# Optimization experiments

Hardware: AMD Instinct MI355X
Metric: run time of the kernel (lower is better)

Reference implementation:

```python
import jax, jax.numpy as jnp
import numpy as np

B, N, M, D = 16, 1024, 1024, 768


def setup_inputs() -> dict:
    key = jax.random.key(0)
    k1, k2, k3, k4, k5 = jax.random.split(key, 5)
    inp = jax.random.normal(k1, (B, N, D), dtype=jnp.float32)
    mem = jax.random.normal(k2, (B, M, D), dtype=jnp.float32)
    mask = jax.random.randint(k3, (B, M), 0, 2, dtype=jnp.int32)
    w_in = jax.random.normal(k4, (D,), dtype=jnp.float32) * (1.0 / D ** 0.5)
    dot_scale = jax.random.uniform(k5, (D,), dtype=jnp.float32, maxval=1.0 / D ** 0.5)
    return {"input": inp, "memory": mem, "mask": mask, "w_in": w_in, "dot_scale": dot_scale}


def reference(input, memory, mask, w_in, dot_scale):
    # input_dot: Linear(D->1, no bias) -> [B, N]
    input_dot = jnp.einsum('bnd,d->bn', input, w_in)
    # cross_dot: (input * dot_scale) @ memory^T -> [B, N, M]
    cross_dot = jnp.einsum('bnd,bmd->bnm', input * dot_scale, memory)
    att = input_dot[:, :, None] + cross_dot
    # mask: [B, M] broadcast over N; 1e30 * (1 - mask) kills masked positions
    att = att - 1e30 * (1.0 - mask[:, None, :].astype(att.dtype))
    weight_one = jax.nn.softmax(att, axis=-1)
    output_one = jnp.einsum('bnm,bmd->bnd', weight_one, memory)
    return jnp.concatenate([input, output_one], axis=-1)
```

## Files before the change

kernel.cpp:

```cpp
#include <hip/hip_runtime.h>


#define B_ 16
#define N_ 1024
#define M_ 1024
#define D_ 768

#define BN 64
#define BM 128
#define NW 8
#define QSTR 776
#define PSTR 136

typedef __attribute__((ext_vector_type(8))) short short8;
typedef __attribute__((ext_vector_type(4))) float f32x4;

__device__ __forceinline__ unsigned short f2bf(float x) {
    unsigned int u = __builtin_bit_cast(unsigned int, x);
    u += 0x7FFFu + ((u >> 16) & 1u);
    return (unsigned short)(u >> 16);
}
__device__ __forceinline__ unsigned pack2(float a, float b) {
    return (unsigned)f2bf(a) | ((unsigned)f2bf(b) << 16);
}

__global__ __launch_bounds__(256)
void gather_kernel(const float* __restrict__ memory,
                   const int* __restrict__ mask,
                   unsigned short* __restrict__ km,
                   unsigned short* __restrict__ kmT)
{
    int blk = blockIdx.x;
    int b   = blk & 15;
    int rem = blk >> 4;
    int mt  = rem / 12;
    int dt  = rem - mt * 12;
    int tid  = threadIdx.x;
    int lane = tid & 63;
    int wv   = tid >> 6;

    __shared__ int wt[4];
    __shared__ int loc[64];

    int4 mv = ((const int4*)(mask + b * M_))[tid];
    int tsum = mv.x + mv.y + mv.z + mv.w;
    int x = tsum;
#pragma unroll
    for (int d = 1; d < 64; d <<= 1) {
        int u = __shfl_up(x, d);
        if (lane >= d) x += u;
    }
    if (lane == 63) wt[wv] = x;
    __syncthreads();
    int cnt = wt[0] + wt[1] + wt[2] + wt[3];
    int m0  = mt * 64;
    int Mp  = ((cnt + BM - 1) / BM) * BM;
    if (m0 >= Mp) return;

    int base = 0;
    for (int w2 = 0; w2 < wv; ++w2) base += wt[w2];
    int p  = base + x - tsum;
    int m1 = m0 + 64;
    if (mv.x) { if (p >= m0 && p < m1) loc[p - m0] = 4 * tid + 0; p++; }
    if (mv.y) { if (p >= m0 && p < m1) loc[p - m0] = 4 * tid + 1; p++; }
    if (mv.z) { if (p >= m0 && p < m1) loc[p - m0] = 4 * tid + 2; p++; }
    if (mv.w) { if (p >= m0 && p < m1) loc[p - m0] = 4 * tid + 3; p++; }
    __syncthreads();

    int c = tid & 15, g = tid >> 4;
    int d0 = dt * 64 + g * 4;
    const float* mem_b = memory + (size_t)b * M_ * D_;
    float v[4][4];
#pragma unroll
    for (int r = 0; r < 4; ++r) {
        int j = m0 + 4 * c + r;
        if (j < cnt) {
            const f32x4* sp = (const f32x4*)(mem_b + (size_t)loc[4 * c + r] * D_ + d0);
            f32x4 t = __builtin_nontemporal_load(sp);
            v[r][0] = t.x; v[r][1] = t.y; v[r][2] = t.z; v[r][3] = t.w;
        } else {
            v[r][0] = v[r][1] = v[r][2] = v[r][3] = 0.f;
        }
    }
    unsigned short* km_b  = km  + (size_t)b * M_ * D_;
    unsigned short* kmT_b = kmT + (size_t)b * D_ * M_;
#pragma unroll
    for (int r = 0; r < 4; ++r) {
        uint2 pk; pk.x = pack2(v[r][0], v[r][1]); pk.y = pack2(v[r][2], v[r][3]);
        *(uint2*)(km_b + (size_t)(m0 + 4 * c + r) * D_ + d0) = pk;
    }
#pragma unroll
    for (int rr = 0; rr < 4; ++rr) {
        uint2 pk; pk.x = pack2(v[0][rr], v[1][rr]); pk.y = pack2(v[2][rr], v[3][rr]);
        *(uint2*)(kmT_b + (size_t)(d0 + rr) * M_ + m0 + 4 * c) = pk;
    }
}

__global__ __launch_bounds__(512, 2)
void attn_kernel(const float* __restrict__ input,
                 const int* __restrict__ mask,
                 const float* __restrict__ dot_scale,
                 const unsigned short* __restrict__ km,
                 const unsigned short* __restrict__ kmT,
                 float* __restrict__ out)
{
    int wg   = blockIdx.x;
    int b    = wg & 15;
    int n0   = (wg >> 4) * BN;
    int tid  = threadIdx.x;
    int wv   = tid >> 6;
    int lane = tid & 63;
    int quad = lane >> 4;
    int l16  = lane & 15;

    __shared__ __align__(16) unsigned short q_lds[BN * QSTR];
    __shared__ __align__(16) unsigned short p_lds[2 * BN * PSTR];
    __shared__ __align__(16) float wsum[BN * NW];
    __shared__ int wt[NW];

    {
        int2 mv = ((const int2*)(mask + b * M_))[tid];
        int ms = mv.x + mv.y;
#pragma unroll
        for (int d2 = 1; d2 < 64; d2 <<= 1) ms += __shfl_xor(ms, d2);
        if (lane == 0) wt[wv] = ms;
    }

    const float* inp_b = input + ((size_t)b * N_ + n0) * D_;
    float*       out_b = out + ((size_t)b * N_ + n0) * (2 * D_);

    {
        int srow = tid >> 3;
        int si   = tid & 7;
        const f32x4* inrow  = (const f32x4*)(inp_b + (size_t)srow * D_);
        f32x4*       outrow = (f32x4*)(out_b + (size_t)srow * 2 * D_);
        unsigned short* qrow = q_lds + srow * QSTR;
        const f32x4* dsv = (const f32x4*)dot_scale;
#pragma unroll 4
        for (int it = 0; it < 24; ++it) {
            int c4 = si + 8 * it;
            f32x4 v = __builtin_nontemporal_load(inrow + c4);
            __builtin_nontemporal_store(v, outrow + c4);
            f32x4 ds = dsv[c4];
            uint2 pk; pk.x = pack2(v.x * ds.x, v.y * ds.y); pk.y = pack2(v.z * ds.z, v.w * ds.w);
            *(uint2*)(qrow + c4 * 4) = pk;
        }
    }
    __syncthreads();
    int cnt = 0;
#pragma unroll
    for (int w2 = 0; w2 < NW; ++w2) cnt += wt[w2];
    int nc = (cnt + BM - 1) / BM;

    f32x4 acc[4][6];
#pragma unroll
    for (int rf = 0; rf < 4; ++rf)
#pragma unroll
        for (int df = 0; df < 6; ++df)
            acc[rf][df] = (f32x4){0.f, 0.f, 0.f, 0.f};
    float psum[4][4];
#pragma unroll
    for (int rf = 0; rf < 4; ++rf)
#pragma unroll
        for (int r = 0; r < 4; ++r) psum[rf][r] = 0.f;

    const unsigned short* km_b  = km  + (size_t)b * M_ * D_;
    const unsigned short* kmT_b = kmT + (size_t)b * D_ * M_;

    for (int ch = 0; ch < nc; ++ch) {
        int m0 = ch * BM;
        const unsigned short* vb = kmT_b + (size_t)(wv * 96 + l16) * M_ + m0 + quad * 8;

        f32x4 s[4];
        s[0] = s[1] = s[2] = s[3] = (f32x4){0.f, 0.f, 0.f, 0.f};
        {
            const unsigned short* kb = km_b + (size_t)(m0 + wv * 16 + l16) * D_ + quad * 8;
#pragma unroll
            for (int kc = 0; kc < 24; ++kc) {
                short8 bv = *(const short8*)(kb + kc * 32);
#pragma unroll
                for (int rf = 0; rf < 4; ++rf) {
                    short8 av = *(const short8*)(q_lds + (size_t)(rf * 16 + l16) * QSTR + quad * 8 + kc * 32);
                    s[rf] = __builtin_amdgcn_mfma_f32_16x16x32_bf16(av, bv, s[rf], 0, 0, 0);
                }
            }
        }

        short8 vpre0[6], vpre1[6];
#pragma unroll
        for (int df = 0; df < 6; ++df) {
            vpre0[df] = *(const short8*)(vb + (size_t)df * 16 * M_);
            vpre1[df] = *(const short8*)(vb + (size_t)df * 16 * M_ + 32);
        }

        {
            bool valid = (m0 + wv * 16 + l16) < cnt;
            unsigned short* pb = p_lds + (ch & 1) * (BN * PSTR) + wv * 16 + l16;
#pragma unroll
            for (int rf = 0; rf < 4; ++rf)
#pragma unroll
                for (int r = 0; r < 4; ++r) {
                    float p = valid ? __expf(s[rf][r]) : 0.f;
                    psum[rf][r] += p;
                    pb[(size_t)(rf * 16 + quad * 4 + r) * PSTR] = f2bf(p);
                }
        }

        asm volatile("s_waitcnt lgkmcnt(0)" ::: "memory");
        __builtin_amdgcn_s_barrier();
        asm volatile("" ::: "memory");

        {
            const unsigned short* pbase = p_lds + (ch & 1) * (BN * PSTR);
            short8 pa[4];
#pragma unroll
            for (int rf = 0; rf < 4; ++rf)
                pa[rf] = *(const short8*)(pbase + (size_t)(rf * 16 + l16) * PSTR + quad * 8);
#pragma unroll
            for (int df = 0; df < 6; ++df)
#pragma unroll
                for (int rf = 0; rf < 4; ++rf)
                    acc[rf][df] = __builtin_amdgcn_mfma_f32_16x16x32_bf16(pa[rf], vpre0[df], acc[rf][df], 0, 0, 0);
#pragma unroll
            for (int rf = 0; rf < 4; ++rf)
                pa[rf] = *(const short8*)(pbase + (size_t)(rf * 16 + l16) * PSTR + quad * 8 + 32);
#pragma unroll
            for (int df = 0; df < 6; ++df)
#pragma unroll
                for (int rf = 0; rf < 4; ++rf)
                    acc[rf][df] = __builtin_amdgcn_mfma_f32_16x16x32_bf16(pa[rf], vpre1[df], acc[rf][df], 0, 0, 0);
#pragma unroll
            for (int kc = 2; kc < 4; ++kc) {
#pragma unroll
                for (int rf = 0; rf < 4; ++rf)
                    pa[rf] = *(const short8*)(pbase + (size_t)(rf * 16 + l16) * PSTR + quad * 8 + kc * 32);
#pragma unroll
                for (int df = 0; df < 6; ++df) {
                    short8 bv = *(const short8*)(vb + (size_t)df * 16 * M_ + kc * 32);
#pragma unroll
                    for (int rf = 0; rf < 4; ++rf)
                        acc[rf][df] = __builtin_amdgcn_mfma_f32_16x16x32_bf16(pa[rf], bv, acc[rf][df], 0, 0, 0);
                }
            }
        }
    }

#pragma unroll
    for (int rf = 0; rf < 4; ++rf)
#pragma unroll
        for (int r = 0; r < 4; ++r) {
            float t = psum[rf][r];
            t += __shfl_xor(t, 1);
            t += __shfl_xor(t, 2);
            t += __shfl_xor(t, 4);
            t += __shfl_xor(t, 8);
            if (l16 == 0) wsum[(rf * 16 + quad * 4 + r) * NW + wv] = t;
        }
    __syncthreads();

#pragma unroll
    for (int rf = 0; rf < 4; ++rf) {
        float li[4];
#pragma unroll
        for (int r = 0; r < 4; ++r) {
            const f32x4* wp = (const f32x4*)&wsum[(rf * 16 + quad * 4 + r) * NW];
            f32x4 w0 = wp[0], w1 = wp[1];
            li[r] = 1.f / (w0.x + w0.y + w0.z + w0.w + w1.x + w1.y + w1.z + w1.w);
        }
#pragma unroll
        for (int df = 0; df < 6; ++df) {
            int col = D_ + wv * 96 + df * 16 + l16;
#pragma unroll
            for (int r = 0; r < 4; ++r)
                __builtin_nontemporal_store(acc[rf][df][r] * li[r],
                    out_b + (size_t)(rf * 16 + quad * 4 + r) * (2 * D_) + col);
        }
    }
}

extern "C" void kernel_launch(void* const* d_in, const int* in_sizes, int n_in,
                              void* d_out, int out_size, void* d_ws, size_t ws_size,
                              hipStream_t stream)
{
    const float* input     = (const float*)d_in[0];
    const float* memory    = (const float*)d_in[1];
    const int*   mask      = (const int*)d_in[2];
    const float* dot_scale = (const float*)d_in[4];
    float* out = (float*)d_out;

    unsigned short* km  = (unsigned short*)d_ws;
    unsigned short* kmT = km + (size_t)B_ * M_ * D_;

    gather_kernel<<<dim3(16 * 12 * B_), dim3(256), 0, stream>>>(memory, mask, km, kmT);
    attn_kernel<<<dim3(B_ * (N_ / BN)), dim3(512), 0, stream>>>(input, mask, dot_scale, km, kmT, out);
}
```

Before: 239.2 us.

## Software-pipeline K and V global loads across chunks with register prefetch

Keeps eight K fragments in registers, rotating prefetches through the 24-step QK loop, and issues the first loads of the next chunk during the current one. V fragments are loaded one k-slice ahead of their MFMA use in the PV stage rather than in a blocking loop. The aim is to hide global-memory latency behind MFMA work. The trade-off is higher register pressure, which could reduce occupancy or cause spills.

```diff
diff --git a/kernel.cpp b/kernel.cpp
--- a/kernel.cpp
+++ b/kernel.cpp
@@ -118,6 +118,15 @@
     __shared__ __align__(16) float wsum[BN * NW];
     __shared__ int wt[NW];
 
+    const unsigned short* km_b  = km  + (size_t)b * M_ * D_;
+    const unsigned short* kmT_b = kmT + (size_t)b * D_ * M_;
+    const unsigned short* kbase = km_b + (size_t)(wv * 16 + l16) * D_ + quad * 8;
+    const unsigned short* vbase = kmT_b + (size_t)(wv * 96 + l16) * M_ + quad * 8;
+
+    short8 kpre[8];
+#pragma unroll
+    for (int i = 0; i < 8; ++i) kpre[i] = *(const short8*)(kbase + i * 32);
+
     {
         int2 mv = ((const int2*)(mask + b * M_))[tid];
         int ms = mv.x + mv.y;
@@ -164,33 +173,50 @@
 #pragma unroll
         for (int r = 0; r < 4; ++r) psum[rf][r] = 0.f;
 
-    const unsigned short* km_b  = km  + (size_t)b * M_ * D_;
-    const unsigned short* kmT_b = kmT + (size_t)b * D_ * M_;
-
     for (int ch = 0; ch < nc; ++ch) {
-        int m0 = ch * BM;
-        const unsigned short* vb = kmT_b + (size_t)(wv * 96 + l16) * M_ + m0 + quad * 8;
+        int m0  = ch * BM;
+        int m0n = (ch + 1 < nc) ? m0 + BM : 0;
+        const unsigned short* kb  = kbase + (size_t)m0 * D_;
+        const unsigned short* kbn = kbase + (size_t)m0n * D_;
+        const unsigned short* vb  = vbase + m0;
 
         f32x4 s[4];
         s[0] = s[1] = s[2] = s[3] = (f32x4){0.f, 0.f, 0.f, 0.f};
-        {
-            const unsigned short* kb = km_b + (size_t)(m0 + wv * 16 + l16) * D_ + quad * 8;
-#pragma unroll
-            for (int kc = 0; kc < 24; ++kc) {
-                short8 bv = *(const short8*)(kb + kc * 32);
-#pragma unroll
-                for (int rf = 0; rf < 4; ++rf) {
-                    short8 av = *(const short8*)(q_lds + (size_t)(rf * 16 + l16) * QSTR + quad * 8 + kc * 32);
-                    s[rf] = __builtin_amdgcn_mfma_f32_16x16x32_bf16(av, bv, s[rf], 0, 0, 0);
-                }
+
+        short8 vpre[6];
+#pragma unroll
+        for (int df = 0; df < 6; ++df)
+            vpre[df] = *(const short8*)(vb + (size_t)df * 16 * M_);
+
+#pragma unroll
+        for (int i = 0; i < 8; ++i) {
+            short8 kv = kpre[i];
+            kpre[i] = *(const short8*)(kb + (8 + i) * 32);
+#pragma unroll
+            for (int rf = 0; rf < 4; ++rf) {
+                short8 av = *(const short8*)(q_lds + (size_t)(rf * 16 + l16) * QSTR + quad * 8 + i * 32);
+                s[rf] = __builtin_amdgcn_mfma_f32_16x16x32_bf16(av, kv, s[rf], 0, 0, 0);
             }
         }
-
-        short8 vpre0[6], vpre1[6];
-#pragma unroll
-        for (int df = 0; df < 6; ++df) {
-            vpre0[df] = *(const short8*)(vb + (size_t)df * 16 * M_);
-            vpre1[df] = *(const short8*)(vb + (size_t)df * 16 * M_ + 32);
+#pragma unroll
+        for (int i = 0; i < 8; ++i) {
+            short8 kv = kpre[i];
+            kpre[i] = *(const short8*)(kb + (16 + i) * 32);
+#pragma unroll
+            for (int rf = 0; rf < 4; ++rf) {
+                short8 av = *(const short8*)(q_lds + (size_t)(rf * 16 + l16) * QSTR + quad * 8 + (8 + i) * 32);
+                s[rf] = __builtin_amdgcn_mfma_f32_16x16x32_bf16(av, kv, s[rf], 0, 0, 0);
+            }
+        }
+#pragma unroll
+        for (int i = 0; i < 8; ++i) {
+            short8 kv = kpre[i];
+            kpre[i] = *(const short8*)(kbn + i * 32);
+#pragma unroll
+            for (int rf = 0; rf < 4; ++rf) {
+                short8 av = *(const short8*)(q_lds + (size_t)(rf * 16 + l16) * QSTR + quad * 8 + (16 + i) * 32);
+                s[rf] = __builtin_amdgcn_mfma_f32_16x16x32_bf16(av, kv, s[rf], 0, 0, 0);
+            }
         }
 
         {
@@ -213,6 +239,11 @@
         {
             const unsigned short* pbase = p_lds + (ch & 1) * (BN * PSTR);
             short8 pa[4];
+            short8 v1[6], v2[6], v3[6];
+
+#pragma unroll
+            for (int df = 0; df < 6; ++df)
+                v1[df] = *(const short8*)(vb + (size_t)df * 16 * M_ + 32);
 #pragma unroll
             for (int rf = 0; rf < 4; ++rf)
                 pa[rf] = *(const short8*)(pbase + (size_t)(rf * 16 + l16) * PSTR + quad * 8);
@@ -220,7 +251,10 @@
             for (int df = 0; df < 6; ++df)
 #pragma unroll
                 for (int rf = 0; rf < 4; ++rf)
-                    acc[rf][df] = __builtin_amdgcn_mfma_f32_16x16x32_bf16(pa[rf], vpre0[df], acc[rf][df], 0, 0, 0);
+                    acc[rf][df] = __builtin_amdgcn_mfma_f32_16x16x32_bf16(pa[rf], vpre[df], acc[rf][df], 0, 0, 0);
+#pragma unroll
+            for (int df = 0; df < 6; ++df)
+                v2[df] = *(const short8*)(vb + (size_t)df * 16 * M_ + 64);
 #pragma unroll
             for (int rf = 0; rf < 4; ++rf)
                 pa[rf] = *(const short8*)(pbase + (size_t)(rf * 16 + l16) * PSTR + quad * 8 + 32);
@@ -228,20 +262,26 @@
             for (int df = 0; df < 6; ++df)
 #pragma unroll
                 for (int rf = 0; rf < 4; ++rf)
-                    acc[rf][df] = __builtin_amdgcn_mfma_f32_16x16x32_bf16(pa[rf], vpre1[df], acc[rf][df], 0, 0, 0);
-#pragma unroll
-            for (int kc = 2; kc < 4; ++kc) {
+                    acc[rf][df] = __builtin_amdgcn_mfma_f32_16x16x32_bf16(pa[rf], v1[df], acc[rf][df], 0, 0, 0);
+#pragma unroll
+            for (int df = 0; df < 6; ++df)
+                v3[df] = *(const short8*)(vb + (size_t)df * 16 * M_ + 96);
+#pragma unroll
+            for (int rf = 0; rf < 4; ++rf)
+                pa[rf] = *(const short8*)(pbase + (size_t)(rf * 16 + l16) * PSTR + quad * 8 + 64);
+#pragma unroll
+            for (int df = 0; df < 6; ++df)
 #pragma unroll
                 for (int rf = 0; rf < 4; ++rf)
-                    pa[rf] = *(const short8*)(pbase + (size_t)(rf * 16 + l16) * PSTR + quad * 8 + kc * 32);
-#pragma unroll
-                for (int df = 0; df < 6; ++df) {
-                    short8 bv = *(const short8*)(vb + (size_t)df * 16 * M_ + kc * 32);
-#pragma unroll
-                    for (int rf = 0; rf < 4; ++rf)
-                        acc[rf][df] = __builtin_amdgcn_mfma_f32_16x16x32_bf16(pa[rf], bv, acc[rf][df], 0, 0, 0);
-                }
-            }
+                    acc[rf][df] = __builtin_amdgcn_mfma_f32_16x16x32_bf16(pa[rf], v2[df], acc[rf][df], 0, 0, 0);
+#pragma unroll
+            for (int rf = 0; rf < 4; ++rf)
+                pa[rf] = *(const short8*)(pbase + (size_t)(rf * 16 + l16) * PSTR + quad * 8 + 96);
+#pragma unroll
+            for (int df = 0; df < 6; ++df)
+#pragma unroll
+                for (int rf = 0; rf < 4; ++rf)
+                    acc[rf][df] = __builtin_amdgcn_mfma_f32_16x16x32_bf16(pa[rf], v3[df], acc[rf][df], 0, 0, 0);
         }
     }
 
```

Result: slower. 250.4 us (+4.7%).

## Double key chunk to 256, switch QK^T to 32x32 MFMA, spread input copy

Applied to the files above, without the earlier changes.

Each memory chunk grows from 128 to 256 keys, so every wave now computes a 64x32 score tile with 32x32x16 bf16 MFMAs instead of 16x16x32 ones. The P buffer goes from double-buffered to single-buffered with an extra barrier before it is rewritten. The PV loop runs over 8 k-slices per chunk. The passthrough copy of input into the first half of the output is moved out of the prologue and split across the chunk iterations, so those global stores overlap with compute. This halves the number of loop iterations and barriers and gives more reuse per key load, in exchange for higher register pressure, an added sync, and coarser handling of partly masked chunks.

```diff
diff --git a/kernel.cpp b/kernel.cpp
--- a/kernel.cpp
+++ b/kernel.cpp
@@ -7,13 +7,14 @@
 #define D_ 768
 
 #define BN 64
-#define BM 128
+#define BM 256
 #define NW 8
 #define QSTR 776
-#define PSTR 136
+#define PSTR 264
 
 typedef __attribute__((ext_vector_type(8))) short short8;
 typedef __attribute__((ext_vector_type(4))) float f32x4;
+typedef __attribute__((ext_vector_type(16))) float f32x16;
 
 __device__ __forceinline__ unsigned short f2bf(float x) {
     unsigned int u = __builtin_bit_cast(unsigned int, x);
@@ -112,9 +113,12 @@
     int lane = tid & 63;
     int quad = lane >> 4;
     int l16  = lane & 15;
+    int l31  = lane & 31;
+    int h    = lane >> 5;
+    int h8   = h * 8;
 
     __shared__ __align__(16) unsigned short q_lds[BN * QSTR];
-    __shared__ __align__(16) unsigned short p_lds[2 * BN * PSTR];
+    __shared__ __align__(16) unsigned short p_lds[BN * PSTR];
     __shared__ __align__(16) float wsum[BN * NW];
     __shared__ int wt[NW];
 
@@ -129,18 +133,17 @@
     const float* inp_b = input + ((size_t)b * N_ + n0) * D_;
     float*       out_b = out + ((size_t)b * N_ + n0) * (2 * D_);
 
+    int srow = tid >> 3;
+    int si   = tid & 7;
+    const f32x4* inrow  = (const f32x4*)(inp_b + (size_t)srow * D_);
+    f32x4*       outrow = (f32x4*)(out_b + (size_t)srow * 2 * D_);
     {
-        int srow = tid >> 3;
-        int si   = tid & 7;
-        const f32x4* inrow  = (const f32x4*)(inp_b + (size_t)srow * D_);
-        f32x4*       outrow = (f32x4*)(out_b + (size_t)srow * 2 * D_);
         unsigned short* qrow = q_lds + srow * QSTR;
         const f32x4* dsv = (const f32x4*)dot_scale;
 #pragma unroll 4
         for (int it = 0; it < 24; ++it) {
             int c4 = si + 8 * it;
-            f32x4 v = __builtin_nontemporal_load(inrow + c4);
-            __builtin_nontemporal_store(v, outrow + c4);
+            f32x4 v = inrow[c4];
             f32x4 ds = dsv[c4];
             uint2 pk; pk.x = pack2(v.x * ds.x, v.y * ds.y); pk.y = pack2(v.z * ds.z, v.w * ds.w);
             *(uint2*)(qrow + c4 * 4) = pk;
@@ -150,7 +153,8 @@
     int cnt = 0;
 #pragma unroll
     for (int w2 = 0; w2 < NW; ++w2) cnt += wt[w2];
-    int nc = (cnt + BM - 1) / BM;
+    int nc  = (cnt + BM - 1) / BM;
+    int ncc = nc < 1 ? 1 : nc;
 
     f32x4 acc[4][6];
 #pragma unroll
@@ -158,31 +162,56 @@
 #pragma unroll
         for (int df = 0; df < 6; ++df)
             acc[rf][df] = (f32x4){0.f, 0.f, 0.f, 0.f};
-    float psum[4][4];
-#pragma unroll
-    for (int rf = 0; rf < 4; ++rf)
-#pragma unroll
-        for (int r = 0; r < 4; ++r) psum[rf][r] = 0.f;
+    float psum[2][16];
+#pragma unroll
+    for (int rg = 0; rg < 2; ++rg)
+#pragma unroll
+        for (int r = 0; r < 16; ++r) psum[rg][r] = 0.f;
 
     const unsigned short* km_b  = km  + (size_t)b * M_ * D_;
     const unsigned short* kmT_b = kmT + (size_t)b * D_ * M_;
 
-    for (int ch = 0; ch < nc; ++ch) {
+    for (int ch = 0; ch < ncc; ++ch) {
         int m0 = ch * BM;
         const unsigned short* vb = kmT_b + (size_t)(wv * 96 + l16) * M_ + m0 + quad * 8;
 
-        f32x4 s[4];
-        s[0] = s[1] = s[2] = s[3] = (f32x4){0.f, 0.f, 0.f, 0.f};
+        f32x16 s2[2] = {};
         {
-            const unsigned short* kb = km_b + (size_t)(m0 + wv * 16 + l16) * D_ + quad * 8;
-#pragma unroll
-            for (int kc = 0; kc < 24; ++kc) {
-                short8 bv = *(const short8*)(kb + kc * 32);
-#pragma unroll
-                for (int rf = 0; rf < 4; ++rf) {
-                    short8 av = *(const short8*)(q_lds + (size_t)(rf * 16 + l16) * QSTR + quad * 8 + kc * 32);
-                    s[rf] = __builtin_amdgcn_mfma_f32_16x16x32_bf16(av, bv, s[rf], 0, 0, 0);
+            const unsigned short* kb = km_b + (size_t)(m0 + wv * 32 + l31) * D_ + h8;
+#pragma unroll
+            for (int ks = 0; ks < 48; ++ks) {
+                short8 bv = *(const short8*)(kb + ks * 16);
+#pragma unroll
+                for (int rg = 0; rg < 2; ++rg) {
+                    short8 av = *(const short8*)(q_lds + (size_t)(rg * 32 + l31) * QSTR + h8 + ks * 16);
+                    s2[rg] = __builtin_amdgcn_mfma_f32_32x32x16_bf16(av, bv, s2[rg], 0, 0, 0);
                 }
+            }
+        }
+
+        __builtin_amdgcn_s_barrier();
+        asm volatile("" ::: "memory");
+
+        {
+            bool valid = (m0 + wv * 32 + l31) < cnt;
+            unsigned short* pb = p_lds + wv * 32 + l31;
+#pragma unroll
+            for (int rg = 0; rg < 2; ++rg)
+#pragma unroll
+                for (int r = 0; r < 16; ++r) {
+                    int nloc = rg * 32 + (r & 3) + 8 * (r >> 2) + 4 * h;
+                    float p = valid ? __expf(s2[rg][r]) : 0.f;
+                    psum[rg][r] += p;
+                    pb[(size_t)nloc * PSTR] = f2bf(p);
+                }
+        }
+
+        {
+            int it0 = (24 * ch) / ncc, it1 = (24 * (ch + 1)) / ncc;
+            for (int it = it0; it < it1; ++it) {
+                int c4 = si + 8 * it;
+                f32x4 v = __builtin_nontemporal_load(inrow + c4);
+                __builtin_nontemporal_store(v, outrow + c4);
             }
         }
 
@@ -193,25 +222,12 @@
             vpre1[df] = *(const short8*)(vb + (size_t)df * 16 * M_ + 32);
         }
 
-        {
-            bool valid = (m0 + wv * 16 + l16) < cnt;
-            unsigned short* pb = p_lds + (ch & 1) * (BN * PSTR) + wv * 16 + l16;
-#pragma unroll
-            for (int rf = 0; rf < 4; ++rf)
-#pragma unroll
-                for (int r = 0; r < 4; ++r) {
-                    float p = valid ? __expf(s[rf][r]) : 0.f;
-                    psum[rf][r] += p;
-                    pb[(size_t)(rf * 16 + quad * 4 + r) * PSTR] = f2bf(p);
-                }
-        }
-
         asm volatile("s_waitcnt lgkmcnt(0)" ::: "memory");
         __builtin_amdgcn_s_barrier();
         asm volatile("" ::: "memory");
 
-        {
-            const unsigned short* pbase = p_lds + (ch & 1) * (BN * PSTR);
+        if (ch < nc) {
+            const unsigned short* pbase = p_lds;
             short8 pa[4];
 #pragma unroll
             for (int rf = 0; rf < 4; ++rf)
@@ -230,7 +246,7 @@
                 for (int rf = 0; rf < 4; ++rf)
                     acc[rf][df] = __builtin_amdgcn_mfma_f32_16x16x32_bf16(pa[rf], vpre1[df], acc[rf][df], 0, 0, 0);
 #pragma unroll
-            for (int kc = 2; kc < 4; ++kc) {
+            for (int kc = 2; kc < 8; ++kc) {
 #pragma unroll
                 for (int rf = 0; rf < 4; ++rf)
                     pa[rf] = *(const short8*)(pbase + (size_t)(rf * 16 + l16) * PSTR + quad * 8 + kc * 32);
@@ -246,15 +262,19 @@
     }
 
 #pragma unroll
-    for (int rf = 0; rf < 4; ++rf)
-#pragma unroll
-        for (int r = 0; r < 4; ++r) {
-            float t = psum[rf][r];
+    for (int rg = 0; rg < 2; ++rg)
+#pragma unroll
+        for (int r = 0; r < 16; ++r) {
+            float t = psum[rg][r];
             t += __shfl_xor(t, 1);
             t += __shfl_xor(t, 2);
             t += __shfl_xor(t, 4);
             t += __shfl_xor(t, 8);
-            if (l16 == 0) wsum[(rf * 16 + quad * 4 + r) * NW + wv] = t;
+            t += __shfl_xor(t, 16);
+            if (l31 == 0) {
+                int nloc = rg * 32 + (r & 3) + 8 * (r >> 2) + 4 * h;
+                wsum[nloc * NW + wv] = t;
+            }
         }
     __syncthreads();
 
```

Measured after the change: 276.9 us. 1.16x slower.
